# Performance work log

Measured on AMD Instinct MI355X. Metric: run time of the kernel, lower is better.

The kernel has to match this reference:

```python
import jax, jax.numpy as jnp
import numpy as np

# Model constants (match init_kwargs)
B, V, NUM_NODES, NUM_RELS = 32, 20, 4000, 400
EMB, HID, L, N, E, OUT = 128, 128, 3, 32000, 256000, 128
DECAY = 0.03
EPS = 0.0  # self_attn eps, not trained


def setup_inputs() -> dict:
    key = jax.random.key(0)
    ks = jax.random.split(key, 20)
    s = 0.02
    return {
        "node_ids": jax.random.randint(ks[0], (N,), 0, NUM_NODES),
        "rel_ids": jax.random.randint(ks[1], (E,), 0, NUM_RELS),
        "edge_index": jax.random.randint(ks[2], (2, E), 0, N),
        "batch": jnp.sort(jax.random.randint(ks[3], (N,), 0, B)),
        "visit_node": jax.random.uniform(ks[4], (B, V, NUM_NODES), dtype=jnp.float32),
        "ehr_nodes": jax.random.uniform(ks[5], (B, NUM_NODES), dtype=jnp.float32),
        "node_emb": jax.random.normal(ks[6], (NUM_NODES, EMB), dtype=jnp.float32) * s,
        "rel_emb": jax.random.normal(ks[7], (NUM_RELS, EMB), dtype=jnp.float32) * s,
        "lin_w": jax.random.normal(ks[8], (HID, EMB), dtype=jnp.float32) * s,
        "lin_b": jnp.zeros((HID,), jnp.float32),
        "alpha_w": jax.random.normal(ks[9], (L, NUM_NODES, NUM_NODES), dtype=jnp.float32) * 0.002,
        "alpha_b": jnp.zeros((L, NUM_NODES), jnp.float32),
        "beta_w": jax.random.normal(ks[10], (L, 1, NUM_NODES), dtype=jnp.float32) * s,
        "beta_b": jnp.zeros((L, 1), jnp.float32),
        "wr_w": jax.random.normal(ks[11], (L, 1, HID), dtype=jnp.float32) * s,
        "wr_b": jnp.zeros((L, 1), jnp.float32),
        "nn_w": jax.random.normal(ks[12], (L, HID, HID), dtype=jnp.float32) * s,
        "nn_b": jnp.zeros((L, HID), jnp.float32),
        "mlp_w": jax.random.normal(ks[13], (OUT, 2 * HID), dtype=jnp.float32) * s,
        "mlp_b": jnp.zeros((OUT,), jnp.float32),
    }


def reference(node_ids, rel_ids, edge_index, batch, visit_node, ehr_nodes,
              node_emb, rel_emb, lin_w, lin_b, alpha_w, alpha_b, beta_w, beta_b,
              wr_w, wr_b, nn_w, nn_b, mlp_w, mlp_b):
    # visit decay weights lambda_j: (1, V, 1)
    lambda_j = jnp.exp(DECAY * (V - jnp.arange(V, dtype=jnp.float32))).reshape(1, V, 1)

    x = node_emb[node_ids] @ lin_w.T + lin_b          # (N, HID)
    edge_attr = rel_emb[rel_ids] @ lin_w.T + lin_b    # (E, HID)
    src, dst = edge_index[0], edge_index[1]
    nid_src = node_ids[src]
    b_src = batch[src]

    for l in range(L):
        # alpha: softmax over visit dim, (B, V, NUM_NODES)
        alpha = jax.nn.softmax(
            jnp.einsum('bvn,mn->bvm', visit_node, alpha_w[l]) + alpha_b[l], axis=1)
        # beta: (B, V, 1) with visit decay
        beta = jnp.tanh(
            jnp.einsum('bvn,on->bvo', visit_node, beta_w[l]) + beta_b[l]) * lambda_j
        attn = jnp.sum(alpha * beta, axis=1)          # (B, NUM_NODES)
        e_attn = attn[b_src, nid_src][:, None]        # (E, 1) per-edge attention

        # BiAttentionGNNConv message: relu(x_j * attn + W_R(edge_attr) * edge_attr)
        w_rel = edge_attr @ wr_w[l].T + wr_b[l]       # (E, 1)
        msg = jax.nn.relu(x[src] * e_attn + w_rel * edge_attr)
        agg = jax.ops.segment_sum(msg, dst, num_segments=N)  # scatter-add aggregate
        out = agg + (1.0 + EPS) * x                   # eps residual
        x = jax.nn.relu(out @ nn_w[l].T + nn_b[l])    # conv.nn Linear + outer relu

    # graph-level patient embedding: global mean pool over batch
    counts = jnp.maximum(
        jax.ops.segment_sum(jnp.ones((N, 1), x.dtype), batch, num_segments=B), 1.0)
    x_graph = jax.ops.segment_sum(x, batch, num_segments=B) / counts  # (B, HID)

    # node-level patient embedding: ehr multihot average of node embeddings
    x_node = (ehr_nodes @ node_emb) / jnp.sum(ehr_nodes, axis=1, keepdims=True)
    x_node = x_node @ lin_w.T + lin_b                 # (B, HID)

    logits = jnp.concatenate([x_graph, x_node], axis=1) @ mlp_w.T + mlp_b
    return logits
```

## Files before the change

### kernel.cpp

```cpp
#include <hip/hip_runtime.h>

namespace {

constexpr int kNodes = 4000;
constexpr int kRels  = 400;
constexpr int kB     = 32;
constexpr int kV     = 20;
constexpr int kN     = 32000;
constexpr int kE     = 256000;
constexpr int kH     = 128;
constexpr int kL     = 3;
constexpr int kMPad  = 4096;
constexpr int kKW    = 4000;
constexpr int kBV    = kB * kV;
constexpr int kNB    = 32;
constexpr int kChunk = kE / kNB;
constexpr int kHalf  = 16000;
constexpr int kPSeg  = 16;
constexpr int kESeg  = 32;

typedef __attribute__((ext_vector_type(8))) short bf16x8;
typedef __attribute__((ext_vector_type(4))) float f32x4;

__device__ inline unsigned short f2bf(float f){
  unsigned int u = __float_as_uint(f);
  u += 0x7FFFu + ((u >> 16) & 1u);
  return (unsigned short)(u >> 16);
}
__device__ inline float bf2f(unsigned short u){
  return __uint_as_float(((unsigned int)u) << 16);
}

__device__ inline void gload_lds16(const unsigned short* g, unsigned short* l){
  __builtin_amdgcn_global_load_lds(
      (const __attribute__((address_space(1))) unsigned int*)(g),
      (__attribute__((address_space(3))) unsigned int*)(l),
      16, 0, 0);
}


__global__ void transpose_kernel(const float* __restrict__ lin_w, const float* __restrict__ nn_w,
                                 float* __restrict__ lin_wT, float* __restrict__ nn_wT){
  int m = blockIdx.x;
  const float* in = (m == 0) ? lin_w : nn_w + (size_t)(m-1)*kH*kH;
  float* out      = (m == 0) ? lin_wT : nn_wT + (size_t)(m-1)*kH*kH;
  for (int i = threadIdx.x; i < kH*kH; i += blockDim.x){
    int r = i >> 7, c = i & (kH-1);
    out[c*kH + r] = in[i];
  }
}

__global__ __launch_bounds__(128) void proj_kernel(const float* __restrict__ node_emb,
    const float* __restrict__ rel_emb, const float* __restrict__ lin_wT,
    const float* __restrict__ lin_b, float* __restrict__ emb_lin, float* __restrict__ rel_lin){
  int row = blockIdx.x;
  const float* src; float* dst;
  if (row < kNodes){ src = node_emb + (size_t)row*kH; dst = emb_lin + (size_t)row*kH; }
  else             { src = rel_emb + (size_t)(row-kNodes)*kH; dst = rel_lin + (size_t)(row-kNodes)*kH; }
  __shared__ float rs[kH];
  int h = threadIdx.x;
  rs[h] = src[h];
  __syncthreads();
  float acc = lin_b[h];
#pragma unroll 8
  for (int k = 0; k < kH; k++) acc = fmaf(rs[k], lin_wT[k*kH + h], acc);
  dst[h] = acc;
}

__global__ void gather_x0_kernel(const int* __restrict__ node_ids,
                                 const float* __restrict__ emb_lin, float* __restrict__ x,
                                 unsigned short* __restrict__ xbf){
  int idx = blockIdx.x*256 + threadIdx.x;
  if (idx < kN*kH){
    int i = idx >> 7, c = idx & (kH-1);
    float v = emb_lin[(size_t)node_ids[i]*kH + c];
    x[idx] = v;
    xbf[idx] = f2bf(v);
  }
}

__global__ __launch_bounds__(128) void relterm_kernel(const float* __restrict__ rel_lin,
    const float* __restrict__ wr_w, const float* __restrict__ wr_b, float* __restrict__ relterm){
  int l = blockIdx.x / kRels, r = blockIdx.x % kRels;
  int t = threadIdx.x;
  float rl = rel_lin[(size_t)r*kH + t];
  __shared__ float red[kH];
  red[t] = rl * wr_w[l*kH + t];
  __syncthreads();
  for (int o = 64; o > 0; o >>= 1){
    if (t < o) red[t] += red[t+o];
    __syncthreads();
  }
  float w = red[0] + wr_b[l];
  relterm[((size_t)l*kRels + r)*kH + t] = w * rl;
}


__global__ __launch_bounds__(256) void csr_hist_kernel(const int* __restrict__ dst,
    unsigned short* __restrict__ rank, unsigned int* __restrict__ hpart){
  __shared__ unsigned int hb[kHalf];
  int p = blockIdx.x;
  int base = blockIdx.y * kHalf;
  int t = threadIdx.x;
  for (int i = t; i < kHalf; i += 256) hb[i] = 0u;
  __syncthreads();
  for (int i = t; i < kChunk; i += 256){
    int e = p*kChunk + i;
    int d = dst[e];
    int rel = d - base;
    if ((unsigned)rel < (unsigned)kHalf){
      rank[e] = (unsigned short)atomicAdd(&hb[rel], 1u);
    }
  }
  __syncthreads();
  for (int i = t; i < kHalf; i += 256)
    hpart[(size_t)p*kN + base + i] = hb[i];
}

__global__ __launch_bounds__(256) void csr_col_kernel(unsigned int* __restrict__ hpart,
    int* __restrict__ deg){
  int bin = blockIdx.x*256 + threadIdx.x;
  if (bin >= kN) return;
  unsigned int s = 0;
#pragma unroll
  for (int p = 0; p < kNB; p++){
    size_t idx = (size_t)p*kN + bin;
    unsigned int v = hpart[idx];
    hpart[idx] = s;
    s += v;
  }
  deg[bin] = (int)s;
}

__global__ __launch_bounds__(256) void scanA_kernel(const int* __restrict__ deg,
    int* __restrict__ starts, int* __restrict__ bsum){
  __shared__ int buf[256];
  int gid = blockIdx.x*256 + threadIdx.x;
  int t = threadIdx.x;
  int v = (gid < kN) ? deg[gid] : 0;
  buf[t] = v;
  __syncthreads();
  for (int o = 1; o < 256; o <<= 1){
    int add = (t >= o) ? buf[t-o] : 0;
    __syncthreads();
    buf[t] += add;
    __syncthreads();
  }
  if (gid < kN) starts[gid] = buf[t] - v;
  if (t == 255) bsum[blockIdx.x] = buf[255];
}

__global__ __launch_bounds__(128) void scanB_kernel(const int* __restrict__ bsum,
    int* __restrict__ boffs, int nblk){
  __shared__ int buf[128];
  int t = threadIdx.x;
  int v = (t < nblk) ? bsum[t] : 0;
  buf[t] = v;
  __syncthreads();
  for (int o = 1; o < 128; o <<= 1){
    int add = (t >= o) ? buf[t-o] : 0;
    __syncthreads();
    buf[t] += add;
    __syncthreads();
  }
  if (t < nblk) boffs[t] = buf[t] - v;
}

__global__ __launch_bounds__(256) void scanC_kernel(int* __restrict__ starts,
    const int* __restrict__ boffs){
  int gid = blockIdx.x*256 + threadIdx.x;
  if (gid < kN) starts[gid] += boffs[blockIdx.x];
  if (gid == kN-1) starts[kN] = kE;
}

__global__ __launch_bounds__(256) void csr_place_kernel(const int* __restrict__ dst,
    const int* __restrict__ src, const int* __restrict__ rel_ids,
    const int* __restrict__ starts, const unsigned int* __restrict__ colOff,
    const unsigned short* __restrict__ rank,
    int* __restrict__ src_perm, int* __restrict__ rel_perm){
  int blk = blockIdx.x;
  int p = blk >> 2;
  for (int i = threadIdx.x; i < 2000; i += 256){
    int e = blk*2000 + i;
    int d = dst[e];
    int pos = starts[d] + (int)colOff[(size_t)p*kN + d] + (int)rank[e];
    src_perm[pos] = src[e];
    rel_perm[pos] = rel_ids[e];
  }
}

__global__ void ub_kernel(const int* __restrict__ batch, int* __restrict__ ub){
  int j = threadIdx.x;
  if (j > kB) return;
  int lo = 0, hi = kN;
  while (lo < hi){
    int mid = (lo + hi) >> 1;
    if (batch[mid] < j) lo = mid + 1; else hi = mid;
  }
  ub[j] = lo;
}


__global__ __launch_bounds__(256) void visit_prep_kernel(const float* __restrict__ visit,
    const float* __restrict__ beta_w, const float* __restrict__ beta_b,
    unsigned short* __restrict__ visitbf, float* __restrict__ beta){
  int bv = blockIdx.x;
  int t = threadIdx.x;
  const float* row = visit + (size_t)bv*kKW;
  unsigned short* outr = visitbf + (size_t)bv*kKW;
  float d0 = 0.f, d1 = 0.f, d2 = 0.f;
  for (int i = t; i < kKW/4; i += 256){
    float4 v = *reinterpret_cast<const float4*>(row + i*4);
    unsigned int lo = ((unsigned int)f2bf(v.y) << 16) | f2bf(v.x);
    unsigned int hi = ((unsigned int)f2bf(v.w) << 16) | f2bf(v.z);
    *reinterpret_cast<uint2*>(outr + i*4) = uint2{lo, hi};
    float4 w0 = *reinterpret_cast<const float4*>(beta_w + i*4);
    float4 w1 = *reinterpret_cast<const float4*>(beta_w + kKW + i*4);
    float4 w2 = *reinterpret_cast<const float4*>(beta_w + 2*kKW + i*4);
    d0 = fmaf(v.x,w0.x, fmaf(v.y,w0.y, fmaf(v.z,w0.z, fmaf(v.w,w0.w, d0))));
    d1 = fmaf(v.x,w1.x, fmaf(v.y,w1.y, fmaf(v.z,w1.z, fmaf(v.w,w1.w, d1))));
    d2 = fmaf(v.x,w2.x, fmaf(v.y,w2.y, fmaf(v.z,w2.z, fmaf(v.w,w2.w, d2))));
  }
#pragma unroll
  for (int o = 32; o > 0; o >>= 1){
    d0 += __shfl_down(d0, o);
    d1 += __shfl_down(d1, o);
    d2 += __shfl_down(d2, o);
  }
  __shared__ float part[3][4];
  int wv = t >> 6, ln = t & 63;
  if (ln == 0){ part[0][wv] = d0; part[1][wv] = d1; part[2][wv] = d2; }
  __syncthreads();
  if (t < 3){
    float s = part[t][0] + part[t][1] + part[t][2] + part[t][3];
    int v = bv % kV;
    float lam = __expf(0.03f * (float)(kV - v));
    beta[t*kBV + bv] = tanhf(s + beta_b[t]) * lam;
  }
}

__global__ void cvtW_kernel(const float* __restrict__ W, unsigned short* __restrict__ out){
  int i = blockIdx.x*256 + threadIdx.x;
  constexpr int perL = kMPad*(kKW/8);
  if (i >= kL*perL) return;
  int l = i / perL;
  int rem = i - l*perL;
  int row = rem / (kKW/8);
  int col = (rem - row*(kKW/8)) * 8;
  unsigned short r[8];
  if (row < kNodes){
    const float* p = W + (size_t)l*kNodes*kNodes + (size_t)row*kKW + col;
    const float4 a = *reinterpret_cast<const float4*>(p);
    const float4 b = *reinterpret_cast<const float4*>(p + 4);
    r[0]=f2bf(a.x); r[1]=f2bf(a.y); r[2]=f2bf(a.z); r[3]=f2bf(a.w);
    r[4]=f2bf(b.x); r[5]=f2bf(b.y); r[6]=f2bf(b.z); r[7]=f2bf(b.w);
  } else {
    for (int q = 0; q < 8; q++) r[q] = 0;
  }
  *reinterpret_cast<uint4*>(out + (size_t)l*kMPad*kKW + (size_t)row*kKW + col)
      = *reinterpret_cast<uint4*>(r);
}

__global__ __launch_bounds__(256) void gemm_bt_bf16(const unsigned short* __restrict__ A,
    const unsigned short* __restrict__ Ball, unsigned short* __restrict__ Sbase){
  __shared__ unsigned short As[2][128*32];
  __shared__ unsigned short Bs[2][128*32];
  int wg = (blockIdx.x & 7)*120 + (blockIdx.x >> 3);
  int lz = wg / 160;
  int rem = wg - lz*160;
  int bn = rem / 5;
  int bm = rem - bn*5;
  int l = lz >> 1, z = lz & 1;
  const unsigned short* B = Ball + (size_t)l*kMPad*kKW;
  unsigned short* C = Sbase + (size_t)lz*kBV*kMPad;
  int tile0 = z ? 63 : 0;
  int nt    = z ? 62 : 63;

  int t = threadIdx.x;
  int lane = t & 63, wave = t >> 6;
  int wm = (wave >> 1) * 64, wn = (wave & 1) * 64;
  int r = lane & 15, g = lane >> 4;

  int ri = lane >> 2, s = lane & 3;
  int koff = ((s ^ ((ri >> 1) & 3)) << 3);
  const unsigned short* Ag = A + (size_t)(bm*128 + wave*32 + ri)*kKW + tile0*32 + koff;
  const unsigned short* Bg = B + (size_t)(bn*128 + wave*32 + ri)*kKW + tile0*32 + koff;
  const size_t rstep = (size_t)16*kKW;

  f32x4 acc[4][4];
#pragma unroll
  for (int i = 0; i < 4; i++)
#pragma unroll
    for (int j = 0; j < 4; j++) acc[i][j] = f32x4{0.f,0.f,0.f,0.f};

  auto STAGE = [&](int buf, int ts){
    const unsigned short* a = Ag + ts*32;
    const unsigned short* b = Bg + ts*32;
    gload_lds16(a,         &As[buf][(wave*32     )*32]);
    gload_lds16(a + rstep, &As[buf][(wave*32 + 16)*32]);
    gload_lds16(b,         &Bs[buf][(wave*32     )*32]);
    gload_lds16(b + rstep, &Bs[buf][(wave*32 + 16)*32]);
  };

  STAGE(0, 0);
  for (int ts = 0; ts < nt; ts++){
    int cur = ts & 1;
    __syncthreads();
    if (ts + 1 < nt) STAGE(cur ^ 1, ts + 1);
    bf16x8 af[4], bf[4];
#pragma unroll
    for (int i = 0; i < 4; i++){
      int arow = wm + i*16 + r;
      int brow = wn + i*16 + r;
      af[i] = *reinterpret_cast<const bf16x8*>(
          &As[cur][arow*32 + ((g ^ ((arow >> 1) & 3)) << 3)]);
      bf[i] = *reinterpret_cast<const bf16x8*>(
          &Bs[cur][brow*32 + ((g ^ ((brow >> 1) & 3)) << 3)]);
    }
#pragma unroll
    for (int i = 0; i < 4; i++)
#pragma unroll
      for (int j = 0; j < 4; j++)
        acc[i][j] = __builtin_amdgcn_mfma_f32_16x16x32_bf16(af[i], bf[j], acc[i][j], 0, 0, 0);
  }
#pragma unroll
  for (int i = 0; i < 4; i++)
#pragma unroll
    for (int j = 0; j < 4; j++){
      int row = bm*128 + wm + i*16 + g*4;
      int col = bn*128 + wn + j*16 + r;
#pragma unroll
      for (int q = 0; q < 4; q++)
        C[(size_t)(row + q)*kMPad + col] = f2bf(acc[i][j][q]);
    }
}

__global__ __launch_bounds__(256) void attn_kernel(const unsigned short* __restrict__ S,
    const float* __restrict__ beta, float* __restrict__ attn){
  int idx = blockIdx.x*256 + threadIdx.x;
  if (idx >= kL*kB*kNodes) return;
  int l = idx / (kB*kNodes);
  int rem = idx - l*(kB*kNodes);
  int b = rem / kNodes;
  int m = rem - b*kNodes;
  const unsigned short* S0 = S + (size_t)(l*2)*kBV*kMPad + (size_t)b*kV*kMPad + m;
  const unsigned short* S1 = S0 + (size_t)kBV*kMPad;
  float vals[kV];
  float mx = -1e30f;
#pragma unroll
  for (int v = 0; v < kV; v++){
    float s = bf2f(S0[(size_t)v*kMPad]) + bf2f(S1[(size_t)v*kMPad]);
    vals[v] = s; mx = fmaxf(mx, s);
  }
  float se = 0.f, ws = 0.f;
  const float* bp = beta + l*kBV + b*kV;
#pragma unroll
  for (int v = 0; v < kV; v++){ float e = __expf(vals[v] - mx); se += e; ws = fmaf(e, bp[v], ws); }
  attn[idx] = ws / se;
}

__global__ void att_e_kernel(const int* __restrict__ src_perm, const int* __restrict__ batch,
    const int* __restrict__ node_ids, const float* __restrict__ attn,
    float* __restrict__ att_e){
  int idx = blockIdx.x*256 + threadIdx.x;
  if (idx >= kL*kE) return;
  int l = idx / kE, p = idx - l*kE;
  int s = src_perm[p];
  att_e[idx] = attn[(size_t)l*kB*kNodes + (size_t)batch[s]*kNodes + node_ids[s]];
}


__global__ __launch_bounds__(512) void aggnn_kernel(const int* __restrict__ starts,
    const int* __restrict__ src_perm, const int* __restrict__ rel_perm,
    const float* __restrict__ att_e_l, const float* __restrict__ relterm_l,
    const unsigned short* __restrict__ xbf_in, unsigned short* __restrict__ xbf_out,
    float* __restrict__ x, const float* __restrict__ nn_wT_l, const float* __restrict__ nn_b_l){
  __shared__ float rows[8][kH];
  int t = threadIdx.x;
  int wv = t >> 6, lane = t & 63;
  int node = blockIdx.x*8 + wv;
  int p0 = starts[node], p1 = starts[node+1];
  int c = lane*2;
  float a0 = 0.f, a1 = 0.f;

  float at_c = 0.f;
  unsigned int xv_c = 0u;
  float2 rt_c = float2{0.f, 0.f};
  if (p0 < p1){
    int s0 = src_perm[p0], r0 = rel_perm[p0];
    at_c = att_e_l[p0];
    xv_c = *reinterpret_cast<const unsigned int*>(&xbf_in[(size_t)s0*kH + c]);
    rt_c = *reinterpret_cast<const float2*>(&relterm_l[(size_t)r0*kH + c]);
  }
  for (int p = p0; p < p1; p++){
    float at_n = 0.f;
    unsigned int xv_n = 0u;
    float2 rt_n = float2{0.f, 0.f};
    if (p + 1 < p1){
      int sn = src_perm[p+1], rn = rel_perm[p+1];
      at_n = att_e_l[p+1];
      xv_n = *reinterpret_cast<const unsigned int*>(&xbf_in[(size_t)sn*kH + c]);
      rt_n = *reinterpret_cast<const float2*>(&relterm_l[(size_t)rn*kH + c]);
    }
    float x0 = __uint_as_float(xv_c << 16);
    float x1 = __uint_as_float(xv_c & 0xFFFF0000u);
    float m0 = fmaf(x0, at_c, rt_c.x); m0 = m0 > 0.f ? m0 : 0.f;
    float m1 = fmaf(x1, at_c, rt_c.y); m1 = m1 > 0.f ? m1 : 0.f;
    a0 += m0; a1 += m1;
    at_c = at_n; xv_c = xv_n; rt_c = rt_n;
  }
  size_t gi = (size_t)node*kH + c;
  rows[wv][c]   = a0 + x[gi];
  rows[wv][c+1] = a1 + x[gi+1];
  __syncthreads();
  int cc = t & 127;
  int r0 = (t >> 7) * 2;
  float acc0 = 0.f, acc1 = 0.f;
#pragma unroll 8
  for (int k = 0; k < kH; k++){
    float w = nn_wT_l[k*kH + cc];
    acc0 = fmaf(rows[r0  ][k], w, acc0);
    acc1 = fmaf(rows[r0+1][k], w, acc1);
  }
  float b = nn_b_l[cc];
  float o0 = fmaxf(acc0 + b, 0.f);
  float o1 = fmaxf(acc1 + b, 0.f);
  size_t n0 = (size_t)(blockIdx.x*8 + r0)*kH + cc;
  x[n0]        = o0;  xbf_out[n0]        = f2bf(o0);
  x[n0 + kH]   = o1;  xbf_out[n0 + kH]   = f2bf(o1);
}

__global__ __launch_bounds__(128) void readprep_kernel(const float* __restrict__ x,
    const int* __restrict__ ub, const float* __restrict__ ehr,
    const float* __restrict__ node_emb, float* __restrict__ pp,
    float* __restrict__ pn, float* __restrict__ ps){
  int s = blockIdx.x, b = blockIdx.y, c = threadIdx.x;
  if (s < kPSeg){
    int lo = ub[b], len = ub[b+1] - lo;
    int i0 = lo + (int)(((long long)len * s) / kPSeg);
    int i1 = lo + (int)(((long long)len * (s+1)) / kPSeg);
    float acc = 0.f;
    for (int i = i0; i < i1; i++) acc += x[(size_t)i*kH + c];
    pp[(size_t)(b*kPSeg + s)*kH + c] = acc;
  } else {
    int q = s - kPSeg;
    constexpr int seg = kNodes/kESeg;
    int n0 = q * seg;
    const float* ep = ehr + (size_t)b*kNodes + n0;
    const float* ne = node_emb + (size_t)n0*kH + c;
    float acc0 = 0.f, acc1 = 0.f, es = 0.f;
#pragma unroll 4
    for (int n = 0; n < seg - 1; n += 2){
      float e0 = ep[n], e1 = ep[n+1];
      es += e0 + e1;
      acc0 = fmaf(e0, ne[(size_t)n*kH], acc0);
      acc1 = fmaf(e1, ne[(size_t)(n+1)*kH], acc1);
    }
    {
      float e0 = ep[seg - 1];
      es += e0;
      acc0 = fmaf(e0, ne[(size_t)(seg - 1)*kH], acc0);
    }
    pn[(size_t)(b*kESeg + q)*kH + c] = acc0 + acc1;
    if (c == 0) ps[b*kESeg + q] = es;
  }
}

__global__ __launch_bounds__(128) void readout_kernel(const float* __restrict__ pp,
    const int* __restrict__ ub, const float* __restrict__ pn, const float* __restrict__ ps,
    const float* __restrict__ lin_wT, const float* __restrict__ lin_b,
    const float* __restrict__ mlp_w, const float* __restrict__ mlp_b,
    float* __restrict__ out){
  int b = blockIdx.x, h = threadIdx.x;
  __shared__ float v[2*kH];
  __shared__ float ts[kH];
  float s = 0.f;
#pragma unroll
  for (int q = 0; q < kPSeg; q++) s += pp[(size_t)(b*kPSeg + q)*kH + h];
  int len = ub[b+1] - ub[b]; if (len < 1) len = 1;
  v[h] = s / (float)len;
  float acc = 0.f, es = 0.f;
#pragma unroll
  for (int q = 0; q < kESeg; q++){
    acc += pn[(size_t)(b*kESeg + q)*kH + h];
    es  += ps[b*kESeg + q];
  }
  ts[h] = acc / es;
  __syncthreads();
  float r = lin_b[h];
#pragma unroll 8
  for (int k = 0; k < kH; k++) r = fmaf(ts[k], lin_wT[k*kH + h], r);
  v[kH + h] = r;
  __syncthreads();
  float o = mlp_b[h];
#pragma unroll 8
  for (int k = 0; k < 2*kH; k++) o = fmaf(v[k], mlp_w[(size_t)h*2*kH + k], o);
  out[b*kH + h] = o;
}

}

extern "C" void kernel_launch(void* const* d_in, const int* in_sizes, int n_in,
                              void* d_out, int out_size, void* d_ws, size_t ws_size,
                              hipStream_t stream){
  const int*   node_ids = (const int*)d_in[0];
  const int*   rel_ids  = (const int*)d_in[1];
  const int*   e_src    = (const int*)d_in[2];
  const int*   e_dst    = e_src + kE;
  const int*   batch    = (const int*)d_in[3];
  const float* visit    = (const float*)d_in[4];
  const float* ehr      = (const float*)d_in[5];
  const float* node_emb = (const float*)d_in[6];
  const float* rel_emb  = (const float*)d_in[7];
  const float* lin_w    = (const float*)d_in[8];
  const float* lin_b    = (const float*)d_in[9];
  const float* alpha_w  = (const float*)d_in[10];
  const float* beta_w   = (const float*)d_in[12];
  const float* beta_b   = (const float*)d_in[13];
  const float* wr_w     = (const float*)d_in[14];
  const float* wr_b     = (const float*)d_in[15];
  const float* nn_w     = (const float*)d_in[16];
  const float* nn_b     = (const float*)d_in[17];
  const float* mlp_w    = (const float*)d_in[18];
  const float* mlp_b    = (const float*)d_in[19];
  float* out = (float*)d_out;

  char* w = (char*)d_ws;
  auto alloc = [&](size_t bytes)->char*{
    char* p = w; w += (bytes + 255) & ~(size_t)255; return p;
  };
  int*   starts = (int*)  alloc((size_t)(kN+1)*4);
  int*   deg    = (int*)  alloc((size_t)kN*4);
  int*   bsum   = (int*)  alloc(256*4);
  int*   boffs  = (int*)  alloc(256*4);
  int*   ub     = (int*)  alloc((kB+1)*4);
  int*   src_perm = (int*)alloc((size_t)kE*4);
  int*   rel_perm = (int*)alloc((size_t)kE*4);
  unsigned short* rank = (unsigned short*)alloc((size_t)kE*2);
  unsigned int* hpart  = (unsigned int*)alloc((size_t)kNB*kN*4);
  float* embLin = (float*)alloc((size_t)kNodes*kH*4);
  float* relLin = (float*)alloc((size_t)kRels*kH*4);
  float* relterm= (float*)alloc((size_t)kL*kRels*kH*4);
  float* linwT  = (float*)alloc((size_t)kH*kH*4);
  float* nnwT   = (float*)alloc((size_t)kL*kH*kH*4);
  float* x      = (float*)alloc((size_t)kN*kH*4);
  unsigned short* xbfA = (unsigned short*)alloc((size_t)kN*kH*2);
  unsigned short* xbfB = (unsigned short*)alloc((size_t)kN*kH*2);
  unsigned short* visitbf = (unsigned short*)alloc((size_t)kBV*kKW*2);
  unsigned short* awbf    = (unsigned short*)alloc((size_t)kL*kMPad*kKW*2);
  unsigned short* S       = (unsigned short*)alloc((size_t)kL*2*kBV*kMPad*2);
  float* attn   = (float*)alloc((size_t)kL*kB*kNodes*4);
  float* att_e  = (float*)alloc((size_t)kL*kE*4);
  float* beta   = (float*)alloc((size_t)kL*kBV*4);
  float* pp     = (float*)alloc((size_t)kB*kPSeg*kH*4);
  float* pn     = (float*)alloc((size_t)kB*kESeg*kH*4);
  float* ps     = (float*)alloc((size_t)kB*kESeg*4);
  if ((size_t)(w - (char*)d_ws) > ws_size) return;

  transpose_kernel<<<4, 256, 0, stream>>>(lin_w, nn_w, linwT, nnwT);
  proj_kernel<<<kNodes + kRels, 128, 0, stream>>>(node_emb, rel_emb, linwT, lin_b, embLin, relLin);
  gather_x0_kernel<<<(kN*kH)/256, 256, 0, stream>>>(node_ids, embLin, x, xbfA);
  relterm_kernel<<<kL*kRels, 128, 0, stream>>>(relLin, wr_w, wr_b, relterm);

  csr_hist_kernel<<<dim3(kNB, 2), 256, 0, stream>>>(e_dst, rank, hpart);
  csr_col_kernel<<<(kN+255)/256, 256, 0, stream>>>(hpart, deg);
  scanA_kernel<<<(kN+255)/256, 256, 0, stream>>>(deg, starts, bsum);
  scanB_kernel<<<1, 128, 0, stream>>>(bsum, boffs, (kN+255)/256);
  scanC_kernel<<<(kN+255)/256, 256, 0, stream>>>(starts, boffs);
  csr_place_kernel<<<128, 256, 0, stream>>>(e_dst, e_src, rel_ids, starts, hpart, rank,
                                            src_perm, rel_perm);
  ub_kernel<<<1, 64, 0, stream>>>(batch, ub);

  visit_prep_kernel<<<kBV, 256, 0, stream>>>(visit, beta_w, beta_b, visitbf, beta);
  cvtW_kernel<<<(kL*kMPad*(kKW/8) + 255)/256, 256, 0, stream>>>(alpha_w, awbf);
  gemm_bt_bf16<<<960, 256, 0, stream>>>(visitbf, awbf, S);
  attn_kernel<<<(kL*kB*kNodes + 255)/256, 256, 0, stream>>>(S, beta, attn);
  att_e_kernel<<<(kL*kE + 255)/256, 256, 0, stream>>>(src_perm, batch, node_ids, attn, att_e);

  unsigned short* xin = xbfA;
  unsigned short* xout = xbfB;
  for (int l = 0; l < kL; l++){
    aggnn_kernel<<<kN/8, 512, 0, stream>>>(starts, src_perm, rel_perm,
        att_e + (size_t)l*kE, relterm + (size_t)l*kRels*kH,
        xin, xout, x, nnwT + (size_t)l*kH*kH, nn_b + (size_t)l*kH);
    unsigned short* tmp = xin; xin = xout; xout = tmp;
  }

  readprep_kernel<<<dim3(kPSeg + kESeg, kB), 128, 0, stream>>>(x, ub, ehr, node_emb, pp, pn, ps);
  readout_kernel<<<kB, 128, 0, stream>>>(pp, ub, pn, ps, linwT, lin_b, mlp_w, mlp_b, out);
}
```

Measured before the change: 519.3 us.

## Pad alpha GEMM K to 4096 and split-K four ways; fuse scan stages

The K dimension of the visit×alpha_w bf16 GEMM is padded from 4000 to 4096 with zero fill, and the split-K factor goes from 2 to 4. This doubles the workgroup count to 1920 so the GPU is better occupied. The attn kernel now sums four bf16 partial results instead of two, which adds output traffic and more bf16 rounding. Separately, the scanB stage is folded into scanC: every block recomputes the block-offset prefix in shared memory, saving one launch.

Measured after the change: 533.9 us. +2.8%, slower.

```diff
diff --git a/kernel.cpp b/kernel.cpp
--- a/kernel.cpp
+++ b/kernel.cpp
@@ -12,6 +12,8 @@
 constexpr int kL     = 3;
 constexpr int kMPad  = 4096;
 constexpr int kKW    = 4000;
+constexpr int kKP    = 4096;
+constexpr int kZS    = 4;
 constexpr int kBV    = kB * kV;
 constexpr int kNB    = 32;
 constexpr int kChunk = kE / kNB;
@@ -150,26 +152,25 @@
   if (t == 255) bsum[blockIdx.x] = buf[255];
 }
 
-__global__ __launch_bounds__(128) void scanB_kernel(const int* __restrict__ bsum,
-    int* __restrict__ boffs, int nblk){
+__global__ __launch_bounds__(256) void scanC_kernel(int* __restrict__ starts,
+    const int* __restrict__ bsum, int nblk){
   __shared__ int buf[128];
   int t = threadIdx.x;
-  int v = (t < nblk) ? bsum[t] : 0;
-  buf[t] = v;
+  if (t < 128){
+    int v = (t < nblk) ? bsum[t] : 0;
+    buf[t] = v;
+  }
   __syncthreads();
   for (int o = 1; o < 128; o <<= 1){
-    int add = (t >= o) ? buf[t-o] : 0;
+    int add = 0;
+    if (t < 128 && t >= o) add = buf[t-o];
     __syncthreads();
-    buf[t] += add;
+    if (t < 128) buf[t] += add;
     __syncthreads();
   }
-  if (t < nblk) boffs[t] = buf[t] - v;
-}
-
-__global__ __launch_bounds__(256) void scanC_kernel(int* __restrict__ starts,
-    const int* __restrict__ boffs){
-  int gid = blockIdx.x*256 + threadIdx.x;
-  if (gid < kN) starts[gid] += boffs[blockIdx.x];
+  int boff = (blockIdx.x > 0) ? buf[blockIdx.x - 1] : 0;
+  int gid = blockIdx.x*256 + t;
+  if (gid < kN) starts[gid] += boff;
   if (gid == kN-1) starts[kN] = kE;
 }
 
@@ -207,19 +208,23 @@
   int bv = blockIdx.x;
   int t = threadIdx.x;
   const float* row = visit + (size_t)bv*kKW;
-  unsigned short* outr = visitbf + (size_t)bv*kKW;
+  unsigned short* outr = visitbf + (size_t)bv*kKP;
   float d0 = 0.f, d1 = 0.f, d2 = 0.f;
-  for (int i = t; i < kKW/4; i += 256){
-    float4 v = *reinterpret_cast<const float4*>(row + i*4);
-    unsigned int lo = ((unsigned int)f2bf(v.y) << 16) | f2bf(v.x);
-    unsigned int hi = ((unsigned int)f2bf(v.w) << 16) | f2bf(v.z);
-    *reinterpret_cast<uint2*>(outr + i*4) = uint2{lo, hi};
-    float4 w0 = *reinterpret_cast<const float4*>(beta_w + i*4);
-    float4 w1 = *reinterpret_cast<const float4*>(beta_w + kKW + i*4);
-    float4 w2 = *reinterpret_cast<const float4*>(beta_w + 2*kKW + i*4);
-    d0 = fmaf(v.x,w0.x, fmaf(v.y,w0.y, fmaf(v.z,w0.z, fmaf(v.w,w0.w, d0))));
-    d1 = fmaf(v.x,w1.x, fmaf(v.y,w1.y, fmaf(v.z,w1.z, fmaf(v.w,w1.w, d1))));
-    d2 = fmaf(v.x,w2.x, fmaf(v.y,w2.y, fmaf(v.z,w2.z, fmaf(v.w,w2.w, d2))));
+  for (int i = t; i < kKP/4; i += 256){
+    if (i*4 < kKW){
+      float4 v = *reinterpret_cast<const float4*>(row + i*4);
+      unsigned int lo = ((unsigned int)f2bf(v.y) << 16) | f2bf(v.x);
+      unsigned int hi = ((unsigned int)f2bf(v.w) << 16) | f2bf(v.z);
+      *reinterpret_cast<uint2*>(outr + i*4) = uint2{lo, hi};
+      float4 w0 = *reinterpret_cast<const float4*>(beta_w + i*4);
+      float4 w1 = *reinterpret_cast<const float4*>(beta_w + kKW + i*4);
+      float4 w2 = *reinterpret_cast<const float4*>(beta_w + 2*kKW + i*4);
+      d0 = fmaf(v.x,w0.x, fmaf(v.y,w0.y, fmaf(v.z,w0.z, fmaf(v.w,w0.w, d0))));
+      d1 = fmaf(v.x,w1.x, fmaf(v.y,w1.y, fmaf(v.z,w1.z, fmaf(v.w,w1.w, d1))));
+      d2 = fmaf(v.x,w2.x, fmaf(v.y,w2.y, fmaf(v.z,w2.z, fmaf(v.w,w2.w, d2))));
+    } else {
+      *reinterpret_cast<uint2*>(outr + i*4) = uint2{0u, 0u};
+    }
   }
 #pragma unroll
   for (int o = 32; o > 0; o >>= 1){
@@ -241,14 +246,14 @@
 
 __global__ void cvtW_kernel(const float* __restrict__ W, unsigned short* __restrict__ out){
   int i = blockIdx.x*256 + threadIdx.x;
-  constexpr int perL = kMPad*(kKW/8);
+  constexpr int perL = kMPad*(kKP/8);
   if (i >= kL*perL) return;
   int l = i / perL;
   int rem = i - l*perL;
-  int row = rem / (kKW/8);
-  int col = (rem - row*(kKW/8)) * 8;
+  int row = rem / (kKP/8);
+  int col = (rem - row*(kKP/8)) * 8;
   unsigned short r[8];
-  if (row < kNodes){
+  if (row < kNodes && col < kKW){
     const float* p = W + (size_t)l*kNodes*kNodes + (size_t)row*kKW + col;
     const float4 a = *reinterpret_cast<const float4*>(p);
     const float4 b = *reinterpret_cast<const float4*>(p + 4);
@@ -257,7 +262,7 @@
   } else {
     for (int q = 0; q < 8; q++) r[q] = 0;
   }
-  *reinterpret_cast<uint4*>(out + (size_t)l*kMPad*kKW + (size_t)row*kKW + col)
+  *reinterpret_cast<uint4*>(out + (size_t)l*kMPad*kKP + (size_t)row*kKP + col)
       = *reinterpret_cast<uint4*>(r);
 }
 
@@ -265,16 +270,16 @@
     const unsigned short* __restrict__ Ball, unsigned short* __restrict__ Sbase){
   __shared__ unsigned short As[2][128*32];
   __shared__ unsigned short Bs[2][128*32];
-  int wg = (blockIdx.x & 7)*120 + (blockIdx.x >> 3);
+  int wg = (blockIdx.x & 7)*240 + (blockIdx.x >> 3);
   int lz = wg / 160;
   int rem = wg - lz*160;
   int bn = rem / 5;
   int bm = rem - bn*5;
-  int l = lz >> 1, z = lz & 1;
-  const unsigned short* B = Ball + (size_t)l*kMPad*kKW;
+  int l = lz >> 2, z = lz & 3;
+  const unsigned short* B = Ball + (size_t)l*kMPad*kKP;
   unsigned short* C = Sbase + (size_t)lz*kBV*kMPad;
-  int tile0 = z ? 63 : 0;
-  int nt    = z ? 62 : 63;
+  int kBase = z * (kKP/kZS);
+  constexpr int nt = (kKP/kZS) / 32;
 
   int t = threadIdx.x;
   int lane = t & 63, wave = t >> 6;
@@ -283,9 +288,9 @@
 
   int ri = lane >> 2, s = lane & 3;
   int koff = ((s ^ ((ri >> 1) & 3)) << 3);
-  const unsigned short* Ag = A + (size_t)(bm*128 + wave*32 + ri)*kKW + tile0*32 + koff;
-  const unsigned short* Bg = B + (size_t)(bn*128 + wave*32 + ri)*kKW + tile0*32 + koff;
-  const size_t rstep = (size_t)16*kKW;
+  const unsigned short* Ag = A + (size_t)(bm*128 + wave*32 + ri)*kKP + kBase + koff;
+  const unsigned short* Bg = B + (size_t)(bn*128 + wave*32 + ri)*kKP + kBase + koff;
+  const size_t rstep = (size_t)16*kKP;
 
   f32x4 acc[4][4];
 #pragma unroll
@@ -343,13 +348,16 @@
   int rem = idx - l*(kB*kNodes);
   int b = rem / kNodes;
   int m = rem - b*kNodes;
-  const unsigned short* S0 = S + (size_t)(l*2)*kBV*kMPad + (size_t)b*kV*kMPad + m;
-  const unsigned short* S1 = S0 + (size_t)kBV*kMPad;
+  const unsigned short* S0 = S + (size_t)(l*kZS)*kBV*kMPad + (size_t)b*kV*kMPad + m;
   float vals[kV];
   float mx = -1e30f;
 #pragma unroll
   for (int v = 0; v < kV; v++){
-    float s = bf2f(S0[(size_t)v*kMPad]) + bf2f(S1[(size_t)v*kMPad]);
+    size_t off = (size_t)v*kMPad;
+    float s = bf2f(S0[off]);
+#pragma unroll
+    for (int z = 1; z < kZS; z++)
+      s += bf2f(S0[(size_t)z*kBV*kMPad + off]);
     vals[v] = s; mx = fmaxf(mx, s);
   }
   float se = 0.f, ws = 0.f;
@@ -532,7 +540,6 @@
   int*   starts = (int*)  alloc((size_t)(kN+1)*4);
   int*   deg    = (int*)  alloc((size_t)kN*4);
   int*   bsum   = (int*)  alloc(256*4);
-  int*   boffs  = (int*)  alloc(256*4);
   int*   ub     = (int*)  alloc((kB+1)*4);
   int*   src_perm = (int*)alloc((size_t)kE*4);
   int*   rel_perm = (int*)alloc((size_t)kE*4);
@@ -546,9 +553,9 @@
   float* x      = (float*)alloc((size_t)kN*kH*4);
   unsigned short* xbfA = (unsigned short*)alloc((size_t)kN*kH*2);
   unsigned short* xbfB = (unsigned short*)alloc((size_t)kN*kH*2);
-  unsigned short* visitbf = (unsigned short*)alloc((size_t)kBV*kKW*2);
-  unsigned short* awbf    = (unsigned short*)alloc((size_t)kL*kMPad*kKW*2);
-  unsigned short* S       = (unsigned short*)alloc((size_t)kL*2*kBV*kMPad*2);
+  unsigned short* visitbf = (unsigned short*)alloc((size_t)kBV*kKP*2);
+  unsigned short* awbf    = (unsigned short*)alloc((size_t)kL*kMPad*kKP*2);
+  unsigned short* S       = (unsigned short*)alloc((size_t)kL*kZS*kBV*kMPad*2);
   float* attn   = (float*)alloc((size_t)kL*kB*kNodes*4);
   float* att_e  = (float*)alloc((size_t)kL*kE*4);
   float* beta   = (float*)alloc((size_t)kL*kBV*4);
@@ -565,15 +572,14 @@
   csr_hist_kernel<<<dim3(kNB, 2), 256, 0, stream>>>(e_dst, rank, hpart);
   csr_col_kernel<<<(kN+255)/256, 256, 0, stream>>>(hpart, deg);
   scanA_kernel<<<(kN+255)/256, 256, 0, stream>>>(deg, starts, bsum);
-  scanB_kernel<<<1, 128, 0, stream>>>(bsum, boffs, (kN+255)/256);
-  scanC_kernel<<<(kN+255)/256, 256, 0, stream>>>(starts, boffs);
+  scanC_kernel<<<(kN+255)/256, 256, 0, stream>>>(starts, bsum, (kN+255)/256);
   csr_place_kernel<<<128, 256, 0, stream>>>(e_dst, e_src, rel_ids, starts, hpart, rank,
                                             src_perm, rel_perm);
   ub_kernel<<<1, 64, 0, stream>>>(batch, ub);
 
   visit_prep_kernel<<<kBV, 256, 0, stream>>>(visit, beta_w, beta_b, visitbf, beta);
-  cvtW_kernel<<<(kL*kMPad*(kKW/8) + 255)/256, 256, 0, stream>>>(alpha_w, awbf);
-  gemm_bt_bf16<<<960, 256, 0, stream>>>(visitbf, awbf, S);
+  cvtW_kernel<<<(kL*kMPad*(kKP/8) + 255)/256, 256, 0, stream>>>(alpha_w, awbf);
+  gemm_bt_bf16<<<1920, 256, 0, stream>>>(visitbf, awbf, S);
   attn_kernel<<<(kL*kB*kNodes + 255)/256, 256, 0, stream>>>(S, beta, attn);
   att_e_kernel<<<(kL*kE + 255)/256, 256, 0, stream>>>(src_perm, batch, node_ids, attn, att_e);
 
```
